# Kernel optimization log

Measured on AMD Instinct MI355X. Metric: run time of the kernel, lower is better.

The kernel has to match this reference:

```python
import jax, jax.numpy as jnp
import numpy as np

N = 50000        # nodes
E = 200000       # edges
D_IN = 128       # dim_input
D_E = 32         # dim_edge_features
D_H = 256        # dim_hidden
D_OUT = 256      # dim_output
N_LAYERS = 3
N_FRAG = 10000
N_GRAPH = 2000
BN_EPS = 1e-5
GINE_EPS = 0.0   # eps buffer, train_eps=False

_LAYER_DIMS = [(D_IN, D_H), (D_H, D_H), (D_H, D_OUT)]  # (node in, node out) per layer


def setup_inputs() -> dict:
    key = jax.random.key(0)
    ks = iter(jax.random.split(key, 64))
    inp = {}
    inp['x'] = jax.random.normal(next(ks), (N, D_IN), dtype=jnp.float32)
    inp['edge_attr'] = jax.random.normal(next(ks), (E, D_E), dtype=jnp.float32)
    inp['edge_index'] = jax.random.randint(next(ks), (2, E), 0, N, dtype=jnp.int64)
    inp['frag_batch'] = jnp.sort(jax.random.randint(next(ks), (N,), 0, N_FRAG, dtype=jnp.int64))
    inp['graph_batch'] = jnp.sort(jax.random.randint(next(ks), (N,), 0, N_GRAPH, dtype=jnp.int64))
    for i, (din, dout) in enumerate(_LAYER_DIMS):
        fin = din + D_E  # MLP input = node feat + edge feat (post-concat message)
        inp[f'w1_{i}'] = jax.random.normal(next(ks), (fin, D_H), dtype=jnp.float32) / np.sqrt(fin)
        inp[f'b1_{i}'] = jnp.zeros((D_H,), dtype=jnp.float32)
        inp[f'w2_{i}'] = jax.random.normal(next(ks), (D_H, dout), dtype=jnp.float32) / np.sqrt(D_H)
        inp[f'b2_{i}'] = jnp.zeros((dout,), dtype=jnp.float32)
        inp[f'g_{i}'] = jnp.ones((dout,), dtype=jnp.float32)     # BN weight
        inp[f'beta_{i}'] = jnp.zeros((dout,), dtype=jnp.float32)  # BN bias
    return inp


def _gine_layer(x, edge_attr, src, dst, w1, b1, w2, b2, g, beta):
    # message: relu(concat(x_j, e_ji)) gathered along edges  -> [E, din+De]
    m = jax.nn.relu(jnp.concatenate([x[src], edge_attr], axis=-1))
    # aggregate: scatter-add into target nodes -> [N, din+De]
    agg = jax.ops.segment_sum(m, dst, num_segments=N)
    # (1+eps)*x residual on the node-feature slice
    agg = agg.at[:, : x.shape[1]].add((1.0 + GINE_EPS) * x)
    # h_Theta MLP: Linear -> ReLU -> Linear
    h = jnp.dot(jax.nn.relu(jnp.dot(agg, w1) + b1), w2) + b2
    # ReLU then BatchNorm1d(track_running_stats=False): batch stats, biased var
    h = jax.nn.relu(h)
    mu = h.mean(axis=0)
    var = h.var(axis=0)
    return g * (h - mu) * jax.lax.rsqrt(var + BN_EPS) + beta


def _sqrt_pool(h, batch, num_segments):
    # nodes_per_graph, broadcast back per-node, sqrt-normalize, then add-pool
    cnt = jax.ops.segment_sum(jnp.ones((h.shape[0],), h.dtype), batch, num_segments=num_segments)
    inv_sqrt = jax.lax.rsqrt(jnp.maximum(cnt, 1.0))[batch]  # [N]
    return jax.ops.segment_sum(h * inv_sqrt[:, None], batch, num_segments=num_segments)


def reference(x, edge_attr, edge_index, frag_batch, graph_batch,
              w1_0, b1_0, w2_0, b2_0, g_0, beta_0,
              w1_1, b1_1, w2_1, b2_1, g_1, beta_1,
              w1_2, b1_2, w2_2, b2_2, g_2, beta_2):
    src, dst = edge_index[0], edge_index[1]
    params = [(w1_0, b1_0, w2_0, b2_0, g_0, beta_0),
              (w1_1, b1_1, w2_1, b2_1, g_1, beta_1),
              (w1_2, b1_2, w2_2, b2_2, g_2, beta_2)]
    h = x
    for p in params:
        h = _gine_layer(h, edge_attr, src, dst, *p)
    frag_out = _sqrt_pool(h, frag_batch, N_FRAG)    # [N_FRAG, D_OUT]
    graph_out = _sqrt_pool(h, graph_batch, N_GRAPH)  # [N_GRAPH, D_OUT]
    return (frag_out, graph_out)
```

## Files before the change

### kernel.cpp

```cpp
#include <hip/hip_runtime.h>

#define N_NODES 50000
#define N_EDGES 200000
#define DE 32
#define N_FRAG 10000
#define N_GRAPH 2000
#define BN_SLOTS 32
#define KSTR 296

typedef _Float16 f16x8 __attribute__((ext_vector_type(8)));
typedef _Float16 f16x4 __attribute__((ext_vector_type(4)));
typedef __attribute__((ext_vector_type(4))) float f32x4;

__device__ __forceinline__ float4 ld4(const float* p) { return *(const float4*)p; }
__device__ __forceinline__ float4 ld4(const _Float16* p) {
    f16x4 h = *(const f16x4*)p;
    float4 v; v.x = (float)h[0]; v.y = (float)h[1]; v.z = (float)h[2]; v.w = (float)h[3];
    return v;
}
__device__ __forceinline__ void st4h(_Float16* p, float4 v) {
    f16x4 h = {(_Float16)v.x, (_Float16)v.y, (_Float16)v.z, (_Float16)v.w};
    *(f16x4*)p = h;
}

__global__ __launch_bounds__(256)
void count_deg_kernel(const int* __restrict__ ei, int* __restrict__ deg) {
    int e = blockIdx.x * 256 + threadIdx.x;
    if (e < N_EDGES) atomicAdd(&deg[ei[N_EDGES + e]], 1);
}

__global__ __launch_bounds__(256)
void block_sum_kernel(const int* __restrict__ deg, int* __restrict__ bsum) {
    int i = blockIdx.x * 256 + threadIdx.x;
    int v = (i < N_NODES) ? deg[i] : 0;
#pragma unroll
    for (int o = 1; o < 64; o <<= 1) v += __shfl_xor(v, o);
    __shared__ int wsum[4];
    if ((threadIdx.x & 63) == 0) wsum[threadIdx.x >> 6] = v;
    __syncthreads();
    if (threadIdx.x == 0) bsum[blockIdx.x] = wsum[0] + wsum[1] + wsum[2] + wsum[3];
}

__global__ __launch_bounds__(256)
void top_scan_kernel(int* __restrict__ bsum, int nb) {
    __shared__ int s[256];
    int t = threadIdx.x;
    s[t] = (t < nb) ? bsum[t] : 0;
    __syncthreads();
    for (int o = 1; o < 256; o <<= 1) {
        int v = s[t];
        int a = (t >= o) ? s[t - o] : 0;
        __syncthreads();
        s[t] = v + a;
        __syncthreads();
    }
    if (t < nb) bsum[t] = (t > 0) ? s[t - 1] : 0;
}

__global__ __launch_bounds__(256)
void final_scan_kernel(const int* __restrict__ deg, const int* __restrict__ bsum,
                       int* __restrict__ ptr) {
    __shared__ int s[256];
    int i = blockIdx.x * 256 + threadIdx.x;
    int t = threadIdx.x;
    int v = (i < N_NODES) ? deg[i] : 0;
    s[t] = v;
    __syncthreads();
    for (int o = 1; o < 256; o <<= 1) {
        int x = s[t];
        int a = (t >= o) ? s[t - o] : 0;
        __syncthreads();
        s[t] = x + a;
        __syncthreads();
    }
    int incl = s[t];
    int base = bsum[blockIdx.x];
    if (i < N_NODES) ptr[i] = base + incl - v;
    if (i == N_NODES - 1) ptr[N_NODES] = base + incl;
}

__global__ __launch_bounds__(256)
void fill_csr_kernel(const int* __restrict__ ei, const int* __restrict__ row_ptr,
                     int* __restrict__ fill, int* __restrict__ csr_src,
                     int* __restrict__ csr_eid) {
    int e = blockIdx.x * 256 + threadIdx.x;
    if (e >= N_EDGES) return;
    int dst = ei[N_EDGES + e];
    int pos = row_ptr[dst] + atomicAdd(&fill[dst], 1);
    csr_src[pos] = ei[e];
    csr_eid[pos] = e;
}

__global__ __launch_bounds__(256)
void segptr_kernel(const int* __restrict__ batch, int nseg, int* __restrict__ ptr) {
    int s = blockIdx.x * 256 + threadIdx.x;
    if (s > nseg) return;
    int lo = 0, hi = N_NODES;
    while (lo < hi) {
        int mid = (lo + hi) >> 1;
        if (batch[mid] < s) lo = mid + 1; else hi = mid;
    }
    ptr[s] = lo;
}

__global__ __launch_bounds__(256)
void bs16_kernel(const float* __restrict__ W, _Float16* __restrict__ BS, int K) {
    int id = blockIdx.x * 256 + threadIdx.x;
    if (id >= K * 256) return;
    int j  = id & 7;
    int l  = (id >> 3) & 63;
    int cg = (id >> 9) & 15;
    int kt = id >> 13;
    int col = cg * 16 + (l & 15);
    int k   = kt * 32 + (l >> 4) * 8 + j;
    BS[id] = (_Float16)W[(size_t)k * 256 + col];
}

__global__ __launch_bounds__(256)
void edge_gather_kernel(const float* __restrict__ ea, const int* __restrict__ row_ptr,
                        const int* __restrict__ csr_eid, float* __restrict__ agg_e) {
    int t = threadIdx.x;
    int g = t >> 3;
    int j = t & 7;
    int n = blockIdx.x * 32 + g;
    if (n >= N_NODES) return;
    int col = j << 2;
    float4 acc = {0.f, 0.f, 0.f, 0.f};
    int beg = row_ptr[n], end = row_ptr[n + 1];
    for (int e = beg; e < end; ++e) {
        int eid = csr_eid[e];
        float4 v = *(const float4*)(ea + (size_t)eid * DE + col);
        acc.x += fmaxf(v.x, 0.f);
        acc.y += fmaxf(v.y, 0.f);
        acc.z += fmaxf(v.z, 0.f);
        acc.w += fmaxf(v.w, 0.f);
    }
    *(float4*)(agg_e + (size_t)n * DE + col) = acc;
}

__global__ __launch_bounds__(256)
void relu16_f32_kernel(const float* __restrict__ x, _Float16* __restrict__ y) {
    size_t i = (size_t)(blockIdx.x * 256 + threadIdx.x) * 4;
    if (i >= (size_t)N_NODES * 128) return;
    float4 v = ld4(x + i);
    f16x4 o = {(_Float16)fmaxf(v.x, 0.f), (_Float16)fmaxf(v.y, 0.f),
               (_Float16)fmaxf(v.z, 0.f), (_Float16)fmaxf(v.w, 0.f)};
    *(f16x4*)(y + i) = o;
}

__global__ __launch_bounds__(256)
void bnrelu16_kernel(const _Float16* __restrict__ h, const float* __restrict__ sc,
                     const float* __restrict__ sh, _Float16* __restrict__ y) {
    size_t i = (size_t)(blockIdx.x * 256 + threadIdx.x) * 8;
    if (i >= (size_t)N_NODES * 256) return;
    int col = (int)(i & 255);
    f16x8 v = *(const f16x8*)(h + i);
    float4 s0 = ld4(sc + col), s1 = ld4(sc + col + 4);
    float4 t0 = ld4(sh + col), t1 = ld4(sh + col + 4);
    f16x8 o;
    o[0] = (_Float16)fmaxf(fmaf((float)v[0], s0.x, t0.x), 0.f);
    o[1] = (_Float16)fmaxf(fmaf((float)v[1], s0.y, t0.y), 0.f);
    o[2] = (_Float16)fmaxf(fmaf((float)v[2], s0.z, t0.z), 0.f);
    o[3] = (_Float16)fmaxf(fmaf((float)v[3], s0.w, t0.w), 0.f);
    o[4] = (_Float16)fmaxf(fmaf((float)v[4], s1.x, t1.x), 0.f);
    o[5] = (_Float16)fmaxf(fmaf((float)v[5], s1.y, t1.y), 0.f);
    o[6] = (_Float16)fmaxf(fmaf((float)v[6], s1.z, t1.z), 0.f);
    o[7] = (_Float16)fmaxf(fmaf((float)v[7], s1.w, t1.w), 0.f);
    *(f16x8*)(y + i) = o;
}

template <bool BNIN, typename T, int NC>
__global__ __launch_bounds__(256, 4)
void fused_mlp_kernel(const T* __restrict__ X, const _Float16* __restrict__ Yg,
                      const int* __restrict__ row_ptr, const int* __restrict__ csr_src,
                      const float* __restrict__ agg_e,
                      const float* __restrict__ bnsc, const float* __restrict__ bnsh,
                      const _Float16* __restrict__ B1, const float* __restrict__ bias1,
                      const _Float16* __restrict__ B2, const float* __restrict__ bias2,
                      _Float16* __restrict__ C, float* __restrict__ bnslot) {
    constexpr int DIN  = NC * 32;
    constexpr int K1   = DIN + 32;
    constexpr int NKT1 = K1 / 32;
    constexpr int CPT  = DIN / 8;
    constexpr int NV   = CPT / 8;
    __shared__ __align__(16) _Float16 sBuf[32 * KSTR];
    const int t = threadIdx.x;
    const int l = t & 63;
    const int w = t >> 6;
    const int lr = l & 15;
    const int lq = l >> 4;
    const int row0 = blockIdx.x << 5;
    const int cb = w << 6;

    {
        const int r = t >> 3, j = t & 7;
        const int gr = row0 + r;
        const int jc = j << 3;
        if (gr < N_NODES) {
            f16x8 acc16[NV];
#pragma unroll
            for (int c = 0; c < NV; ++c) acc16[c] = (f16x8){0, 0, 0, 0, 0, 0, 0, 0};
            const int beg = row_ptr[gr], end = row_ptr[gr + 1];
            for (int e = beg; e < end; ++e) {
                const _Float16* sp = Yg + (size_t)csr_src[e] * DIN + jc;
#pragma unroll
                for (int c = 0; c < NV; ++c) acc16[c] += *(const f16x8*)(sp + c * 64);
            }
            const T* xp = X + (size_t)gr * DIN + jc;
#pragma unroll
            for (int c = 0; c < NV; ++c) {
                float4 v0f = ld4(xp + c * 64);
                float4 v1f = ld4(xp + c * 64 + 4);
                if (BNIN) {
                    float4 sa = *(const float4*)(bnsc + c * 64 + jc);
                    float4 sb = *(const float4*)(bnsc + c * 64 + jc + 4);
                    float4 ta = *(const float4*)(bnsh + c * 64 + jc);
                    float4 tb = *(const float4*)(bnsh + c * 64 + jc + 4);
                    v0f.x = fmaf(v0f.x, sa.x, ta.x);
                    v0f.y = fmaf(v0f.y, sa.y, ta.y);
                    v0f.z = fmaf(v0f.z, sa.z, ta.z);
                    v0f.w = fmaf(v0f.w, sa.w, ta.w);
                    v1f.x = fmaf(v1f.x, sb.x, tb.x);
                    v1f.y = fmaf(v1f.y, sb.y, tb.y);
                    v1f.z = fmaf(v1f.z, sb.z, tb.z);
                    v1f.w = fmaf(v1f.w, sb.w, tb.w);
                }
                f16x8 o;
                o[0] = (_Float16)(v0f.x + (float)acc16[c][0]);
                o[1] = (_Float16)(v0f.y + (float)acc16[c][1]);
                o[2] = (_Float16)(v0f.z + (float)acc16[c][2]);
                o[3] = (_Float16)(v0f.w + (float)acc16[c][3]);
                o[4] = (_Float16)(v1f.x + (float)acc16[c][4]);
                o[5] = (_Float16)(v1f.y + (float)acc16[c][5]);
                o[6] = (_Float16)(v1f.z + (float)acc16[c][6]);
                o[7] = (_Float16)(v1f.w + (float)acc16[c][7]);
                *(f16x8*)&sBuf[r * KSTR + c * 64 + jc] = o;
            }
            float4 ev = *(const float4*)(agg_e + (size_t)gr * DE + (j << 2));
            st4h(&sBuf[r * KSTR + DIN + (j << 2)], ev);
        } else {
            f16x8 z8 = {0, 0, 0, 0, 0, 0, 0, 0};
#pragma unroll
            for (int c = 0; c < NV; ++c)
                *(f16x8*)&sBuf[r * KSTR + c * 64 + jc] = z8;
            f16x4 z4 = {0, 0, 0, 0};
            *(f16x4*)&sBuf[r * KSTR + DIN + (j << 2)] = z4;
        }
    }
    __syncthreads();

    f32x4 acc1[2][4];
#pragma unroll
    for (int mt = 0; mt < 2; ++mt)
#pragma unroll
        for (int nt = 0; nt < 4; ++nt) acc1[mt][nt] = (f32x4){0.f, 0.f, 0.f, 0.f};
#pragma unroll
    for (int kt = 0; kt < NKT1; ++kt) {
        f16x8 af[2], bf[4];
#pragma unroll
        for (int mt = 0; mt < 2; ++mt)
            af[mt] = *(const f16x8*)&sBuf[(mt * 16 + lr) * KSTR + (kt << 5) + (lq << 3)];
        const size_t bb = ((size_t)(kt * 16 + (w << 2))) * 512 + (l << 3);
#pragma unroll
        for (int nt = 0; nt < 4; ++nt)
            bf[nt] = *(const f16x8*)(B1 + bb + nt * 512);
#pragma unroll
        for (int mt = 0; mt < 2; ++mt)
#pragma unroll
            for (int nt = 0; nt < 4; ++nt)
                acc1[mt][nt] = __builtin_amdgcn_mfma_f32_16x16x32_f16(
                    af[mt], bf[nt], acc1[mt][nt], 0, 0, 0);
    }
    __syncthreads();

#pragma unroll
    for (int nt = 0; nt < 4; ++nt) {
        int col = cb + nt * 16 + lr;
        float bv = bias1[col];
#pragma unroll
        for (int mt = 0; mt < 2; ++mt)
#pragma unroll
            for (int i = 0; i < 4; ++i) {
                int rr = mt * 16 + lq * 4 + i;
                sBuf[rr * KSTR + col] = (_Float16)fmaxf(acc1[mt][nt][i] + bv, 0.f);
            }
    }
    __syncthreads();

    f32x4 acc2[2][4];
#pragma unroll
    for (int mt = 0; mt < 2; ++mt)
#pragma unroll
        for (int nt = 0; nt < 4; ++nt) acc2[mt][nt] = (f32x4){0.f, 0.f, 0.f, 0.f};
#pragma unroll
    for (int kt = 0; kt < 8; ++kt) {
        f16x8 af[2], bf[4];
#pragma unroll
        for (int mt = 0; mt < 2; ++mt)
            af[mt] = *(const f16x8*)&sBuf[(mt * 16 + lr) * KSTR + (kt << 5) + (lq << 3)];
        const size_t bb = ((size_t)(kt * 16 + (w << 2))) * 512 + (l << 3);
#pragma unroll
        for (int nt = 0; nt < 4; ++nt)
            bf[nt] = *(const f16x8*)(B2 + bb + nt * 512);
#pragma unroll
        for (int mt = 0; mt < 2; ++mt)
#pragma unroll
            for (int nt = 0; nt < 4; ++nt)
                acc2[mt][nt] = __builtin_amdgcn_mfma_f32_16x16x32_f16(
                    af[mt], bf[nt], acc2[mt][nt], 0, 0, 0);
    }
    __syncthreads();

    float* slot = bnslot + (size_t)(blockIdx.x & (BN_SLOTS - 1)) * 512;
#pragma unroll
    for (int nt = 0; nt < 4; ++nt) {
        int col = cb + nt * 16 + lr;
        float bv = bias2[col];
        float s = 0.f, qq = 0.f;
#pragma unroll
        for (int mt = 0; mt < 2; ++mt)
#pragma unroll
            for (int i = 0; i < 4; ++i) {
                int rr = mt * 16 + lq * 4 + i;
                float o = fmaxf(acc2[mt][nt][i] + bv, 0.f);
                sBuf[rr * KSTR + col] = (_Float16)o;
                if (row0 + rr < N_NODES) { s += o; qq += o * o; }
            }
        s += __shfl_xor(s, 16); s += __shfl_xor(s, 32);
        qq += __shfl_xor(qq, 16); qq += __shfl_xor(qq, 32);
        if (lq == 0) {
            atomicAdd(&slot[col], s);
            atomicAdd(&slot[256 + col], qq);
        }
    }
    __syncthreads();

#pragma unroll
    for (int k = 0; k < 4; ++k) {
        int rr  = (t >> 5) + k * 8;
        int col = (t & 31) * 8;
        int row = row0 + rr;
        if (row < N_NODES) {
            f16x8 v = *(const f16x8*)&sBuf[rr * KSTR + col];
            *(f16x8*)(C + (size_t)row * 256 + col) = v;
        }
    }
}

__global__ void bn_finalize_kernel(const float* __restrict__ slots,
                                   const float* __restrict__ g, const float* __restrict__ beta,
                                   float* __restrict__ scale, float* __restrict__ shift) {
    int c = threadIdx.x;
    float s = 0.f, q = 0.f;
    for (int k = 0; k < BN_SLOTS; ++k) {
        s += slots[(size_t)k * 512 + c];
        q += slots[(size_t)k * 512 + 256 + c];
    }
    float mu = s * (1.0f / N_NODES);
    float var = q * (1.0f / N_NODES) - mu * mu;
    float rstd = rsqrtf(var + 1e-5f);
    float sc = g[c] * rstd;
    scale[c] = sc;
    shift[c] = beta[c] - mu * sc;
}

__global__ __launch_bounds__(256)
void pool_seg_kernel(const _Float16* __restrict__ h, const int* __restrict__ ptr,
                     const float* __restrict__ bnsc, const float* __restrict__ bnsh,
                     float* __restrict__ out, int nseg) {
    int t = threadIdx.x;
    int g = t >> 6;
    int j = t & 63;
    int s = blockIdx.x * 4 + g;
    if (s >= nseg) return;
    int beg = ptr[s], end = ptr[s + 1];
    int col = j << 2;
    float4 sc = *(const float4*)(bnsc + col);
    float4 sh = *(const float4*)(bnsh + col);
    float4 acc = {0.f, 0.f, 0.f, 0.f};
    for (int i = beg; i < end; ++i) {
        float4 v = ld4(h + (size_t)i * 256 + col);
        acc.x += fmaf(v.x, sc.x, sh.x);
        acc.y += fmaf(v.y, sc.y, sh.y);
        acc.z += fmaf(v.z, sc.z, sh.z);
        acc.w += fmaf(v.w, sc.w, sh.w);
    }
    float w = rsqrtf(fmaxf((float)(end - beg), 1.0f));
    float4 o = {acc.x * w, acc.y * w, acc.z * w, acc.w * w};
    *(float4*)(out + (size_t)s * 256 + col) = o;
}

extern "C" void kernel_launch(void* const* d_in, const int* in_sizes, int n_in,
                              void* d_out, int out_size, void* d_ws, size_t ws_size,
                              hipStream_t stream) {
    const float* x  = (const float*)d_in[0];
    const float* ea = (const float*)d_in[1];
    const int*   ei = (const int*)d_in[2];
    const int*   fb = (const int*)d_in[3];
    const int*   gb = (const int*)d_in[4];
    const float* W1[3]   = {(const float*)d_in[5],  (const float*)d_in[11], (const float*)d_in[17]};
    const float* B1[3]   = {(const float*)d_in[6],  (const float*)d_in[12], (const float*)d_in[18]};
    const float* W2[3]   = {(const float*)d_in[7],  (const float*)d_in[13], (const float*)d_in[19]};
    const float* B2[3]   = {(const float*)d_in[8],  (const float*)d_in[14], (const float*)d_in[20]};
    const float* G[3]    = {(const float*)d_in[9],  (const float*)d_in[15], (const float*)d_in[21]};
    const float* BETA[3] = {(const float*)d_in[10], (const float*)d_in[16], (const float*)d_in[22]};

    const int FIN[3] = {160, 288, 288};
    const int NBLK = (N_NODES + 255) / 256;

    float* ws = (float*)d_ws;
    size_t off = 0;
    _Float16* bufA = (_Float16*)(ws + off); off += (size_t)N_NODES * 128;
    _Float16* bufB = (_Float16*)(ws + off); off += (size_t)N_NODES * 128;
    _Float16* ybuf = (_Float16*)(ws + off); off += (size_t)N_NODES * 128;
    float* agg_e = ws + off; off += (size_t)N_NODES * DE;
    float* bnss  = ws + off; off += 3 * 512;
    float* bnslots = ws + off; off += (size_t)3 * BN_SLOTS * 512;
    _Float16* w1f[3]; _Float16* w2f[3];
    {
        _Float16* sw = (_Float16*)(ws + off);
        _Float16* sw0 = sw;
        for (int l = 0; l < 3; ++l) { w1f[l] = sw; sw += 256 * FIN[l]; }
        for (int l = 0; l < 3; ++l) { w2f[l] = sw; sw += 256 * 256; }
        off += (size_t)(sw - sw0 + 1) / 2;
    }
    int* iw      = (int*)(ws + off);
    int* row_ptr = iw;                     iw += N_NODES + 1;
    int* deg     = iw;                     iw += N_NODES;
    int* fill    = iw;                     iw += N_NODES;
    int* csr_src = iw;                     iw += N_EDGES;
    int* csr_eid = iw;                     iw += N_EDGES;
    int* frag_ptr = iw;                    iw += N_FRAG + 1;
    int* graph_ptr = iw;                   iw += N_GRAPH + 1;
    int* bsum    = iw;                     iw += NBLK;

    hipMemsetAsync(deg, 0, 2 * N_NODES * sizeof(int), stream);
    hipMemsetAsync(bnslots, 0, (size_t)3 * BN_SLOTS * 512 * sizeof(float), stream);

    for (int l = 0; l < 3; ++l) {
        bs16_kernel<<<(FIN[l] * 256 + 255) / 256, 256, 0, stream>>>(W1[l], w1f[l], FIN[l]);
        bs16_kernel<<<(256 * 256 + 255) / 256, 256, 0, stream>>>(W2[l], w2f[l], 256);
    }

    count_deg_kernel<<<(N_EDGES + 255) / 256, 256, 0, stream>>>(ei, deg);
    block_sum_kernel<<<NBLK, 256, 0, stream>>>(deg, bsum);
    top_scan_kernel<<<1, 256, 0, stream>>>(bsum, NBLK);
    final_scan_kernel<<<NBLK, 256, 0, stream>>>(deg, bsum, row_ptr);
    fill_csr_kernel<<<(N_EDGES + 255) / 256, 256, 0, stream>>>(ei, row_ptr, fill, csr_src, csr_eid);

    segptr_kernel<<<(N_FRAG + 1 + 255) / 256, 256, 0, stream>>>(fb, N_FRAG, frag_ptr);
    segptr_kernel<<<(N_GRAPH + 1 + 255) / 256, 256, 0, stream>>>(gb, N_GRAPH, graph_ptr);

    edge_gather_kernel<<<(N_NODES + 31) / 32, 256, 0, stream>>>(ea, row_ptr, csr_eid, agg_e);

    const int nblk_mlp = (N_NODES + 31) / 32;
    relu16_f32_kernel<<<(N_NODES * 128 / 4 + 255) / 256, 256, 0, stream>>>(x, ybuf);
    {
        float* slotsL = bnslots;
        fused_mlp_kernel<false, float, 4><<<nblk_mlp, 256, 0, stream>>>(
            x, ybuf, row_ptr, csr_src, agg_e, nullptr, nullptr,
            w1f[0], B1[0], w2f[0], B2[0], bufA, slotsL);
        bn_finalize_kernel<<<1, 256, 0, stream>>>(slotsL, G[0], BETA[0], bnss, bnss + 256);
    }
    {
        float* slotsL = bnslots + (size_t)1 * BN_SLOTS * 512;
        const float* psc = bnss, * psh = bnss + 256;
        bnrelu16_kernel<<<(N_NODES * 256 / 8 + 255) / 256, 256, 0, stream>>>(bufA, psc, psh, ybuf);
        fused_mlp_kernel<true, _Float16, 8><<<nblk_mlp, 256, 0, stream>>>(
            bufA, ybuf, row_ptr, csr_src, agg_e, psc, psh,
            w1f[1], B1[1], w2f[1], B2[1], bufB, slotsL);
        bn_finalize_kernel<<<1, 256, 0, stream>>>(slotsL, G[1], BETA[1], bnss + 512, bnss + 768);
    }
    {
        float* slotsL = bnslots + (size_t)2 * BN_SLOTS * 512;
        const float* psc = bnss + 512, * psh = bnss + 768;
        bnrelu16_kernel<<<(N_NODES * 256 / 8 + 255) / 256, 256, 0, stream>>>(bufB, psc, psh, ybuf);
        fused_mlp_kernel<true, _Float16, 8><<<nblk_mlp, 256, 0, stream>>>(
            bufB, ybuf, row_ptr, csr_src, agg_e, psc, psh,
            w1f[2], B1[2], w2f[2], B2[2], bufA, slotsL);
        bn_finalize_kernel<<<1, 256, 0, stream>>>(slotsL, G[2], BETA[2], bnss + 1024, bnss + 1280);
    }

    const float* fsc = bnss + 2 * 512;
    const float* fsh = fsc + 256;
    pool_seg_kernel<<<(N_FRAG + 3) / 4, 256, 0, stream>>>(bufA, frag_ptr, fsc, fsh,
                                                          (float*)d_out, N_FRAG);
    pool_seg_kernel<<<(N_GRAPH + 3) / 4, 256, 0, stream>>>(bufA, graph_ptr, fsc, fsh,
                                                           (float*)d_out + (size_t)N_FRAG * 256, N_GRAPH);
}
```

Baseline: 376.2 us.

## Double MLP row tile to 64 and merge weight-convert and segptr launches

The fused MLP kernel now processes 64 rows per block instead of 32. Each wave computes four M-tiles, so every B-fragment load from global memory is reused across twice as many rows, and the grid is halved. In addition, the six weight-conversion launches are merged into one kernel, and the two segment-pointer searches are merged into one launch, to cut launch overhead. The larger tile doubles LDS use and accumulator registers, which may lower occupancy under launch_bounds(256,4) and serializes the gather of two row halves per thread.

```diff
diff --git a/kernel.cpp b/kernel.cpp
--- a/kernel.cpp
+++ b/kernel.cpp
@@ -92,9 +92,15 @@
 }
 
 __global__ __launch_bounds__(256)
-void segptr_kernel(const int* __restrict__ batch, int nseg, int* __restrict__ ptr) {
-    int s = blockIdx.x * 256 + threadIdx.x;
-    if (s > nseg) return;
+void segptr2_kernel(const int* __restrict__ fb, const int* __restrict__ gb,
+                    int* __restrict__ frag_ptr, int* __restrict__ graph_ptr) {
+    int id = blockIdx.x * 256 + threadIdx.x;
+    const int* batch;
+    int* ptr;
+    int s;
+    if (id <= N_FRAG) { batch = fb; ptr = frag_ptr; s = id; }
+    else if (id <= N_FRAG + 1 + N_GRAPH) { batch = gb; ptr = graph_ptr; s = id - (N_FRAG + 1); }
+    else return;
     int lo = 0, hi = N_NODES;
     while (lo < hi) {
         int mid = (lo + hi) >> 1;
@@ -103,17 +109,27 @@
     ptr[s] = lo;
 }
 
-__global__ __launch_bounds__(256)
-void bs16_kernel(const float* __restrict__ W, _Float16* __restrict__ BS, int K) {
+struct BsAll {
+    const float* W[6];
+    _Float16* BS[6];
+    int base[7];
+};
+
+__global__ __launch_bounds__(256)
+void bs16_all_kernel(BsAll a) {
     int id = blockIdx.x * 256 + threadIdx.x;
-    if (id >= K * 256) return;
-    int j  = id & 7;
-    int l  = (id >> 3) & 63;
-    int cg = (id >> 9) & 15;
-    int kt = id >> 13;
+    if (id >= a.base[6]) return;
+    int seg = 0;
+#pragma unroll
+    for (int i = 1; i < 6; ++i) seg += (id >= a.base[i]);
+    int lid = id - a.base[seg];
+    int j  = lid & 7;
+    int l  = (lid >> 3) & 63;
+    int cg = (lid >> 9) & 15;
+    int kt = lid >> 13;
     int col = cg * 16 + (l & 15);
     int k   = kt * 32 + (l >> 4) * 8 + j;
-    BS[id] = (_Float16)W[(size_t)k * 256 + col];
+    a.BS[seg][lid] = (_Float16)a.W[seg][(size_t)k * 256 + col];
 }
 
 __global__ __launch_bounds__(256)
@@ -183,89 +199,93 @@
     constexpr int NKT1 = K1 / 32;
     constexpr int CPT  = DIN / 8;
     constexpr int NV   = CPT / 8;
-    __shared__ __align__(16) _Float16 sBuf[32 * KSTR];
+    __shared__ __align__(16) _Float16 sBuf[64 * KSTR];
     const int t = threadIdx.x;
     const int l = t & 63;
     const int w = t >> 6;
     const int lr = l & 15;
     const int lq = l >> 4;
-    const int row0 = blockIdx.x << 5;
+    const int row0 = blockIdx.x << 6;
     const int cb = w << 6;
 
     {
         const int r = t >> 3, j = t & 7;
-        const int gr = row0 + r;
         const int jc = j << 3;
-        if (gr < N_NODES) {
-            f16x8 acc16[NV];
-#pragma unroll
-            for (int c = 0; c < NV; ++c) acc16[c] = (f16x8){0, 0, 0, 0, 0, 0, 0, 0};
-            const int beg = row_ptr[gr], end = row_ptr[gr + 1];
-            for (int e = beg; e < end; ++e) {
-                const _Float16* sp = Yg + (size_t)csr_src[e] * DIN + jc;
-#pragma unroll
-                for (int c = 0; c < NV; ++c) acc16[c] += *(const f16x8*)(sp + c * 64);
+#pragma unroll
+        for (int half = 0; half < 2; ++half) {
+            const int rr = half * 32 + r;
+            const int gr = row0 + rr;
+            if (gr < N_NODES) {
+                f16x8 acc16[NV];
+#pragma unroll
+                for (int c = 0; c < NV; ++c) acc16[c] = (f16x8){0, 0, 0, 0, 0, 0, 0, 0};
+                const int beg = row_ptr[gr], end = row_ptr[gr + 1];
+                for (int e = beg; e < end; ++e) {
+                    const _Float16* sp = Yg + (size_t)csr_src[e] * DIN + jc;
+#pragma unroll
+                    for (int c = 0; c < NV; ++c) acc16[c] += *(const f16x8*)(sp + c * 64);
+                }
+                const T* xp = X + (size_t)gr * DIN + jc;
+#pragma unroll
+                for (int c = 0; c < NV; ++c) {
+                    float4 v0f = ld4(xp + c * 64);
+                    float4 v1f = ld4(xp + c * 64 + 4);
+                    if (BNIN) {
+                        float4 sa = *(const float4*)(bnsc + c * 64 + jc);
+                        float4 sb = *(const float4*)(bnsc + c * 64 + jc + 4);
+                        float4 ta = *(const float4*)(bnsh + c * 64 + jc);
+                        float4 tb = *(const float4*)(bnsh + c * 64 + jc + 4);
+                        v0f.x = fmaf(v0f.x, sa.x, ta.x);
+                        v0f.y = fmaf(v0f.y, sa.y, ta.y);
+                        v0f.z = fmaf(v0f.z, sa.z, ta.z);
+                        v0f.w = fmaf(v0f.w, sa.w, ta.w);
+                        v1f.x = fmaf(v1f.x, sb.x, tb.x);
+                        v1f.y = fmaf(v1f.y, sb.y, tb.y);
+                        v1f.z = fmaf(v1f.z, sb.z, tb.z);
+                        v1f.w = fmaf(v1f.w, sb.w, tb.w);
+                    }
+                    f16x8 o;
+                    o[0] = (_Float16)(v0f.x + (float)acc16[c][0]);
+                    o[1] = (_Float16)(v0f.y + (float)acc16[c][1]);
+                    o[2] = (_Float16)(v0f.z + (float)acc16[c][2]);
+                    o[3] = (_Float16)(v0f.w + (float)acc16[c][3]);
+                    o[4] = (_Float16)(v1f.x + (float)acc16[c][4]);
+                    o[5] = (_Float16)(v1f.y + (float)acc16[c][5]);
+                    o[6] = (_Float16)(v1f.z + (float)acc16[c][6]);
+                    o[7] = (_Float16)(v1f.w + (float)acc16[c][7]);
+                    *(f16x8*)&sBuf[rr * KSTR + c * 64 + jc] = o;
+                }
+                float4 ev = *(const float4*)(agg_e + (size_t)gr * DE + (j << 2));
+                st4h(&sBuf[rr * KSTR + DIN + (j << 2)], ev);
+            } else {
+                f16x8 z8 = {0, 0, 0, 0, 0, 0, 0, 0};
+#pragma unroll
+                for (int c = 0; c < NV; ++c)
+                    *(f16x8*)&sBuf[rr * KSTR + c * 64 + jc] = z8;
+                f16x4 z4 = {0, 0, 0, 0};
+                *(f16x4*)&sBuf[rr * KSTR + DIN + (j << 2)] = z4;
             }
-            const T* xp = X + (size_t)gr * DIN + jc;
-#pragma unroll
-            for (int c = 0; c < NV; ++c) {
-                float4 v0f = ld4(xp + c * 64);
-                float4 v1f = ld4(xp + c * 64 + 4);
-                if (BNIN) {
-                    float4 sa = *(const float4*)(bnsc + c * 64 + jc);
-                    float4 sb = *(const float4*)(bnsc + c * 64 + jc + 4);
-                    float4 ta = *(const float4*)(bnsh + c * 64 + jc);
-                    float4 tb = *(const float4*)(bnsh + c * 64 + jc + 4);
-                    v0f.x = fmaf(v0f.x, sa.x, ta.x);
-                    v0f.y = fmaf(v0f.y, sa.y, ta.y);
-                    v0f.z = fmaf(v0f.z, sa.z, ta.z);
-                    v0f.w = fmaf(v0f.w, sa.w, ta.w);
-                    v1f.x = fmaf(v1f.x, sb.x, tb.x);
-                    v1f.y = fmaf(v1f.y, sb.y, tb.y);
-                    v1f.z = fmaf(v1f.z, sb.z, tb.z);
-                    v1f.w = fmaf(v1f.w, sb.w, tb.w);
-                }
-                f16x8 o;
-                o[0] = (_Float16)(v0f.x + (float)acc16[c][0]);
-                o[1] = (_Float16)(v0f.y + (float)acc16[c][1]);
-                o[2] = (_Float16)(v0f.z + (float)acc16[c][2]);
-                o[3] = (_Float16)(v0f.w + (float)acc16[c][3]);
-                o[4] = (_Float16)(v1f.x + (float)acc16[c][4]);
-                o[5] = (_Float16)(v1f.y + (float)acc16[c][5]);
-                o[6] = (_Float16)(v1f.z + (float)acc16[c][6]);
-                o[7] = (_Float16)(v1f.w + (float)acc16[c][7]);
-                *(f16x8*)&sBuf[r * KSTR + c * 64 + jc] = o;
-            }
-            float4 ev = *(const float4*)(agg_e + (size_t)gr * DE + (j << 2));
-            st4h(&sBuf[r * KSTR + DIN + (j << 2)], ev);
-        } else {
-            f16x8 z8 = {0, 0, 0, 0, 0, 0, 0, 0};
-#pragma unroll
-            for (int c = 0; c < NV; ++c)
-                *(f16x8*)&sBuf[r * KSTR + c * 64 + jc] = z8;
-            f16x4 z4 = {0, 0, 0, 0};
-            *(f16x4*)&sBuf[r * KSTR + DIN + (j << 2)] = z4;
         }
     }
     __syncthreads();
 
-    f32x4 acc1[2][4];
-#pragma unroll
-    for (int mt = 0; mt < 2; ++mt)
+    f32x4 acc1[4][4];
+#pragma unroll
+    for (int mt = 0; mt < 4; ++mt)
 #pragma unroll
         for (int nt = 0; nt < 4; ++nt) acc1[mt][nt] = (f32x4){0.f, 0.f, 0.f, 0.f};
 #pragma unroll
     for (int kt = 0; kt < NKT1; ++kt) {
-        f16x8 af[2], bf[4];
-#pragma unroll
-        for (int mt = 0; mt < 2; ++mt)
+        f16x8 af[4], bf[4];
+#pragma unroll
+        for (int mt = 0; mt < 4; ++mt)
             af[mt] = *(const f16x8*)&sBuf[(mt * 16 + lr) * KSTR + (kt << 5) + (lq << 3)];
         const size_t bb = ((size_t)(kt * 16 + (w << 2))) * 512 + (l << 3);
 #pragma unroll
         for (int nt = 0; nt < 4; ++nt)
             bf[nt] = *(const f16x8*)(B1 + bb + nt * 512);
 #pragma unroll
-        for (int mt = 0; mt < 2; ++mt)
+        for (int mt = 0; mt < 4; ++mt)
 #pragma unroll
             for (int nt = 0; nt < 4; ++nt)
                 acc1[mt][nt] = __builtin_amdgcn_mfma_f32_16x16x32_f16(
@@ -278,7 +298,7 @@
         int col = cb + nt * 16 + lr;
         float bv = bias1[col];
 #pragma unroll
-        for (int mt = 0; mt < 2; ++mt)
+        for (int mt = 0; mt < 4; ++mt)
 #pragma unroll
             for (int i = 0; i < 4; ++i) {
                 int rr = mt * 16 + lq * 4 + i;
@@ -287,23 +307,23 @@
     }
     __syncthreads();
 
-    f32x4 acc2[2][4];
-#pragma unroll
-    for (int mt = 0; mt < 2; ++mt)
+    f32x4 acc2[4][4];
+#pragma unroll
+    for (int mt = 0; mt < 4; ++mt)
 #pragma unroll
         for (int nt = 0; nt < 4; ++nt) acc2[mt][nt] = (f32x4){0.f, 0.f, 0.f, 0.f};
 #pragma unroll
     for (int kt = 0; kt < 8; ++kt) {
-        f16x8 af[2], bf[4];
-#pragma unroll
-        for (int mt = 0; mt < 2; ++mt)
+        f16x8 af[4], bf[4];
+#pragma unroll
+        for (int mt = 0; mt < 4; ++mt)
             af[mt] = *(const f16x8*)&sBuf[(mt * 16 + lr) * KSTR + (kt << 5) + (lq << 3)];
         const size_t bb = ((size_t)(kt * 16 + (w << 2))) * 512 + (l << 3);
 #pragma unroll
         for (int nt = 0; nt < 4; ++nt)
             bf[nt] = *(const f16x8*)(B2 + bb + nt * 512);
 #pragma unroll
-        for (int mt = 0; mt < 2; ++mt)
+        for (int mt = 0; mt < 4; ++mt)
 #pragma unroll
             for (int nt = 0; nt < 4; ++nt)
                 acc2[mt][nt] = __builtin_amdgcn_mfma_f32_16x16x32_f16(
@@ -318,7 +338,7 @@
         float bv = bias2[col];
         float s = 0.f, qq = 0.f;
 #pragma unroll
-        for (int mt = 0; mt < 2; ++mt)
+        for (int mt = 0; mt < 4; ++mt)
 #pragma unroll
             for (int i = 0; i < 4; ++i) {
                 int rr = mt * 16 + lq * 4 + i;
@@ -336,7 +356,7 @@
     __syncthreads();
 
 #pragma unroll
-    for (int k = 0; k < 4; ++k) {
+    for (int k = 0; k < 8; ++k) {
         int rr  = (t >> 5) + k * 8;
         int col = (t & 31) * 8;
         int row = row0 + rr;
@@ -437,9 +457,17 @@
     hipMemsetAsync(deg, 0, 2 * N_NODES * sizeof(int), stream);
     hipMemsetAsync(bnslots, 0, (size_t)3 * BN_SLOTS * 512 * sizeof(float), stream);
 
-    for (int l = 0; l < 3; ++l) {
-        bs16_kernel<<<(FIN[l] * 256 + 255) / 256, 256, 0, stream>>>(W1[l], w1f[l], FIN[l]);
-        bs16_kernel<<<(256 * 256 + 255) / 256, 256, 0, stream>>>(W2[l], w2f[l], 256);
+    {
+        BsAll a;
+        a.W[0] = W1[0]; a.W[1] = W1[1]; a.W[2] = W1[2];
+        a.W[3] = W2[0]; a.W[4] = W2[1]; a.W[5] = W2[2];
+        a.BS[0] = w1f[0]; a.BS[1] = w1f[1]; a.BS[2] = w1f[2];
+        a.BS[3] = w2f[0]; a.BS[4] = w2f[1]; a.BS[5] = w2f[2];
+        int Ks[6] = {FIN[0], FIN[1], FIN[2], 256, 256, 256};
+        int cum = 0;
+        for (int i = 0; i < 6; ++i) { a.base[i] = cum; cum += Ks[i] * 256; }
+        a.base[6] = cum;
+        bs16_all_kernel<<<(cum + 255) / 256, 256, 0, stream>>>(a);
     }
 
     count_deg_kernel<<<(N_EDGES + 255) / 256, 256, 0, stream>>>(ei, deg);
@@ -448,12 +476,12 @@
     final_scan_kernel<<<NBLK, 256, 0, stream>>>(deg, bsum, row_ptr);
     fill_csr_kernel<<<(N_EDGES + 255) / 256, 256, 0, stream>>>(ei, row_ptr, fill, csr_src, csr_eid);
 
-    segptr_kernel<<<(N_FRAG + 1 + 255) / 256, 256, 0, stream>>>(fb, N_FRAG, frag_ptr);
-    segptr_kernel<<<(N_GRAPH + 1 + 255) / 256, 256, 0, stream>>>(gb, N_GRAPH, graph_ptr);
+    segptr2_kernel<<<(N_FRAG + N_GRAPH + 2 + 255) / 256, 256, 0, stream>>>(
+        fb, gb, frag_ptr, graph_ptr);
 
     edge_gather_kernel<<<(N_NODES + 31) / 32, 256, 0, stream>>>(ea, row_ptr, csr_eid, agg_e);
 
-    const int nblk_mlp = (N_NODES + 31) / 32;
+    const int nblk_mlp = (N_NODES + 63) / 64;
     relu16_f32_kernel<<<(N_NODES * 128 / 4 + 255) / 256, 256, 0, stream>>>(x, ybuf);
     {
         float* slotsL = bnslots;
```

Result: faster. 357.0 us (-5.1%).
